# Performance work log

Measured on AMD Instinct MI355X. Metric: run time of the kernel, lower is better.

## Reference

```python
import jax, jax.numpy as jnp
import numpy as np

NEG_SLOPE = 0.01  # F.leaky_relu default


def _unfold3(x):
    # x: [B,C,H,W] -> [B,C,9,H,W] of 3x3 neighborhoods (zero pad 1)
    B, C, H, W = x.shape
    xp = jnp.pad(x, ((0, 0), (0, 0), (1, 1), (1, 1)))
    return jnp.stack([xp[:, :, i:i + H, j:j + W] for i in range(3) for j in range(3)], axis=2)


def _resize_bilinear(img, oh, ow):
    # torch F.interpolate mode='bilinear', align_corners=False, antialias=False
    B, C, H, W = img.shape
    if oh == H and ow == W:
        return img
    def coords(out, inn):
        c = jnp.maximum((jnp.arange(out, dtype=jnp.float32) + 0.5) * (inn / out) - 0.5, 0.0)
        i0 = jnp.floor(c).astype(jnp.int32)
        i1 = jnp.minimum(i0 + 1, inn - 1)
        w = c - i0.astype(jnp.float32)
        return i0, i1, w
    i0, i1, wh = coords(oh, H)
    row = img[:, :, i0, :] * (1.0 - wh)[None, None, :, None] + img[:, :, i1, :] * wh[None, None, :, None]
    j0, j1, ww = coords(ow, W)
    return row[:, :, :, j0] * (1.0 - ww) + row[:, :, :, j1] * ww


def _up2_nearest(x):
    # F.interpolate scale_factor=2 (default mode='nearest')
    return jnp.repeat(jnp.repeat(x, 2, axis=2), 2, axis=3)


def _leaky(x):
    return jnp.where(x >= 0, x, NEG_SLOPE * x)


def _pac_conv(x, guide, w):
    # PacConv2d (gaussian kernel, k=3, stride=1, pad=1, bias=False)
    g_unf = _unfold3(guide)                      # [B,Cg,9,H,W]
    diff = g_unf - guide[:, :, None]             # f_j - f_i
    kern = jnp.exp(-0.5 * jnp.sum(diff * diff, axis=1))  # [B,9,H,W]
    x_unf = _unfold3(x)                          # [B,Ci,9,H,W]
    wk = w.reshape(w.shape[0], w.shape[1], 9)    # [Co,Ci,9]
    return jnp.einsum('oik,bikhw,bkhw->bohw', wk, x_unf, kern)


def setup_inputs() -> dict:
    key = jax.random.key(0)
    ks = jax.random.split(key, 8)
    B, Cx, Hx, Wx = 4, 384, 32, 32
    Hg = Wg = 512
    x = jax.random.normal(ks[0], (B, Cx, Hx, Wx), dtype=jnp.float32)
    guide = jax.random.uniform(ks[1], (B, 3, Hg, Wg), dtype=jnp.float32)
    lin_w = jax.random.normal(ks[2], (16, 384, 1, 1), dtype=jnp.float32) * 0.05
    lin_b = jax.random.normal(ks[3], (16,), dtype=jnp.float32) * 0.05
    chans = [16, 4, 4, 4, 1]
    w0 = jax.random.normal(ks[4], (chans[1], chans[0], 3, 3), dtype=jnp.float32) * 0.1
    w1 = jax.random.normal(ks[5], (chans[2], chans[1], 3, 3), dtype=jnp.float32) * 0.1
    w2 = jax.random.normal(ks[6], (chans[3], chans[2], 3, 3), dtype=jnp.float32) * 0.1
    w3 = jax.random.normal(ks[7], (chans[4], chans[3], 3, 3), dtype=jnp.float32) * 0.1
    return {"x": x, "guide": guide, "lin_w": lin_w, "lin_b": lin_b,
            "w0": w0, "w1": w1, "w2": w2, "w3": w3}


def reference(x, guide, lin_w, lin_b, w0, w1, w2, w3):
    # crop guide to multiple of 16 (module uses shape[-1] for both dims)
    s = (guide.shape[-1] // 16) * 16
    guide = guide[..., :s, :s]
    # 1x1 conv + leaky relu
    x = jnp.einsum('oi,bihw->bohw', lin_w[:, :, 0, 0], x) + lin_b[None, :, None, None]
    x = _leaky(x)
    ws = [w0, w1, w2, w3]
    n = len(ws)
    Hg, Wg = guide.shape[2], guide.shape[3]
    for i in range(n):
        f = 2 ** (n - 1 - i)
        g = _resize_bilinear(guide, Hg // f, Wg // f)
        x = _up2_nearest(x)
        x = _pac_conv(x, g, ws[i])
        if i < n - 1:
            x = _leaky(x)
    return jax.nn.sigmoid(x)
```

## Files before the change

### kernel.cpp

```cpp
#include <hip/hip_runtime.h>
#include <math.h>

#define NEG_SLOPE 0.01f

__device__ inline float bilin(const float* __restrict__ gp, float scale, int r, int c) {
    float ch = fmaxf((r + 0.5f) * scale - 0.5f, 0.f);
    float cw = fmaxf((c + 0.5f) * scale - 0.5f, 0.f);
    int h0 = (int)ch, w0 = (int)cw;
    int h1 = min(h0 + 1, 511), w1 = min(w0 + 1, 511);
    float fh = ch - (float)h0, fw = cw - (float)w0;
    float v00 = gp[h0 * 512 + w0], v01 = gp[h0 * 512 + w1];
    float v10 = gp[h1 * 512 + w0], v11 = gp[h1 * 512 + w1];
    float top = v00 + (v01 - v00) * fw;
    float bot = v10 + (v11 - v10) * fw;
    return top + (bot - top) * fh;
}

__global__ void __launch_bounds__(256)
prep_kernel(const float* __restrict__ x, const float* __restrict__ lw,
            const float* __restrict__ lb, float* __restrict__ x16,
            const float* __restrict__ g, float* __restrict__ g64p,
            float* __restrict__ g128p, float* __restrict__ g256p) {
    int bid = blockIdx.x;
    if (bid < 256) {
        int idx = bid * 256 + threadIdx.x;
        int hw = idx & 1023, co = (idx >> 10) & 15, bb = idx >> 14;
        const float* xp = x + bb * 384 * 1024 + hw;
        const float* wp = lw + co * 384;
        float a0 = 0.f, a1 = 0.f, a2 = 0.f, a3 = 0.f;
        for (int ci = 0; ci < 384; ci += 4) {
            a0 = fmaf(wp[ci],     xp[(ci)     * 1024], a0);
            a1 = fmaf(wp[ci + 1], xp[(ci + 1) * 1024], a1);
            a2 = fmaf(wp[ci + 2], xp[(ci + 2) * 1024], a2);
            a3 = fmaf(wp[ci + 3], xp[(ci + 3) * 1024], a3);
        }
        float acc = lb[co] + ((a0 + a1) + (a2 + a3));
        x16[idx] = acc >= 0.f ? acc : NEG_SLOPE * acc;
    } else {
        int idx = (bid - 256) * 256 + threadIdx.x;
        int R; float scale; float* outp; int o;
        if (idx < 786432)      { R = 256; scale = 2.f; outp = g256p; o = idx; }
        else if (idx < 983040) { R = 128; scale = 4.f; outp = g128p; o = idx - 786432; }
        else                   { R = 64;  scale = 8.f; outp = g64p;  o = idx - 983040; }
        int c = o % R;
        int r = (o / R) % R;
        int bc = o / (R * R);
        outp[o] = bilin(g + (size_t)bc * 262144, scale, r, c);
    }
}

template <int Ci, int Co, int R, int ACT>
__global__ void __launch_bounds__(256)
pac_stage(const float* __restrict__ x, const float* __restrict__ g,
          const float* __restrict__ wk, float* __restrict__ out) {
    __shared__ float sw[Co * Ci * 9];
    for (int i = threadIdx.x; i < Co * Ci * 9; i += 256) sw[i] = wk[i];
    __syncthreads();

    constexpr int HW = R * R;
    constexpr int Rh = R / 2;
    constexpr int HWh = Rh * Rh;
    int idx = blockIdx.x * 256 + threadIdx.x;
    int w = idx & (R - 1);
    int h = (idx / R) & (R - 1);
    int b = idx / HW;

    const float* gb = g + (size_t)b * 3 * HW;
    int ctr = h * R + w;
    float gc0 = gb[ctr];
    float gc1 = gb[HW + ctr];
    float gc2 = gb[2 * HW + ctr];

    float acc[Co];
#pragma unroll
    for (int co = 0; co < Co; ++co) acc[co] = 0.f;

    const float* xb = x + (size_t)b * Ci * HWh;

#pragma unroll
    for (int t = 0; t < 9; ++t) {
        int dh = t / 3 - 1, dw = t % 3 - 1;
        int hh = h + dh, ww = w + dw;
        if (hh < 0 || hh >= R || ww < 0 || ww >= R) continue;
        int tap = hh * R + ww;
        float d0 = gb[tap] - gc0;
        float d1 = gb[HW + tap] - gc1;
        float d2 = gb[2 * HW + tap] - gc2;
        float k = __expf(-0.5f * (d0 * d0 + d1 * d1 + d2 * d2));
        const float* xp = xb + (hh >> 1) * Rh + (ww >> 1);
#pragma unroll
        for (int ci = 0; ci < Ci; ++ci) {
            float xv = xp[ci * HWh] * k;
#pragma unroll
            for (int co = 0; co < Co; ++co)
                acc[co] = fmaf(sw[(co * Ci + ci) * 9 + t], xv, acc[co]);
        }
    }

#pragma unroll
    for (int co = 0; co < Co; ++co) {
        float v = acc[co];
        if (ACT == 0) v = v >= 0.f ? v : NEG_SLOPE * v;
        else          v = 1.0f / (1.0f + __expf(-v));
        out[(size_t)(b * Co + co) * HW + ctr] = v;
    }
}

template <int Ci, int Co>
__device__ inline void pac_lds(const float* __restrict__ sx, int BXr, int BXc, int NX,
                               const float* __restrict__ sg, int BGr, int BGc, int NG,
                               const float* __restrict__ sw, float* __restrict__ so,
                               int BOr, int BOc, int NO, int RES) {
    const int NG2 = NG * NG, NX2 = NX * NX, NO2 = NO * NO;
    for (int i = threadIdx.x; i < NO2; i += 256) {
        int r = i / NO, c = i % NO;
        int gh = BOr + r, gw = BOc + c;
        float acc[Co];
#pragma unroll
        for (int co = 0; co < Co; ++co) acc[co] = 0.f;
        if (gh >= 0 && gh < RES && gw >= 0 && gw < RES) {
            int lc0 = (gh - BGr) * NG + (gw - BGc);
            float gc0 = sg[lc0], gc1 = sg[NG2 + lc0], gc2 = sg[2 * NG2 + lc0];
#pragma unroll
            for (int tt = 0; tt < 9; ++tt) {
                int hh = gh + tt / 3 - 1, ww = gw + tt % 3 - 1;
                if (hh < 0 || hh >= RES || ww < 0 || ww >= RES) continue;
                int lt = (hh - BGr) * NG + (ww - BGc);
                float d0 = sg[lt] - gc0;
                float d1 = sg[NG2 + lt] - gc1;
                float d2 = sg[2 * NG2 + lt] - gc2;
                float k = __expf(-0.5f * (d0 * d0 + d1 * d1 + d2 * d2));
                int lx = ((hh >> 1) - BXr) * NX + ((ww >> 1) - BXc);
#pragma unroll
                for (int ci = 0; ci < Ci; ++ci) {
                    float xv = sx[ci * NX2 + lx] * k;
#pragma unroll
                    for (int co = 0; co < Co; ++co)
                        acc[co] = fmaf(sw[(co * Ci + ci) * 9 + tt], xv, acc[co]);
                }
            }
        }
#pragma unroll
        for (int co = 0; co < Co; ++co) {
            float v = acc[co];
            so[co * NO2 + i] = v >= 0.f ? v : NEG_SLOPE * v;
        }
    }
}

__global__ void __launch_bounds__(256)
pac_tail_kernel(const float* __restrict__ x1g, const float* __restrict__ guide,
                const float* __restrict__ g256p,
                const float* __restrict__ w2, const float* __restrict__ w3,
                float* __restrict__ out) {
    __shared__ float smem[6544];
    float* sw2   = smem;
    float* sw3   = smem + 144;
    float* sg512 = smem + 180;
    float* sg256 = smem + 3648;
    float* sx1   = smem + 4848;
    float* sx2   = smem + 5248;

    int bid = blockIdx.x;
    int xcd = bid & 7;
    int j   = bid >> 3;
    int b    = xcd >> 1;
    int half = xcd & 1;
    int t = half * 8 + (j >> 4);
    int u = j & 15;

    const int B1r = 8 * t - 1,   B1c = 8 * u - 1;
    const int BG2r = 16 * t - 2, BG2c = 16 * u - 2;
    const int B2r = 16 * t - 1,  B2c = 16 * u - 1;
    const int BG3r = 32 * t - 1, BG3c = 32 * u - 1;

    const float* gb = guide + (size_t)b * 3 * 262144;

    for (int i = threadIdx.x; i < 3468; i += 256) {
        int ch = i / 1156, rem = i % 1156, r = rem / 34, c = rem % 34;
        int gr = BG3r + r, gc = BG3c + c;
        float v = 0.f;
        if (gr >= 0 && gr < 512 && gc >= 0 && gc < 512)
            v = gb[ch * 262144 + (gr << 9) + gc];
        sg512[i] = v;
    }
    for (int i = threadIdx.x; i < 1200; i += 256) {
        int ch = i / 400, rem = i % 400, r = rem / 20, c = rem % 20;
        int gr = BG2r + r, gc = BG2c + c;
        float v = 0.f;
        if (gr >= 0 && gr < 256 && gc >= 0 && gc < 256)
            v = g256p[(b * 3 + ch) * 65536 + (gr << 8) + gc];
        sg256[i] = v;
    }
    for (int i = threadIdx.x; i < 400; i += 256) {
        int ci = i / 100, rem = i % 100, r = rem / 10, c = rem % 10;
        int gr = B1r + r, gc = B1c + c;
        float v = 0.f;
        if (gr >= 0 && gr < 128 && gc >= 0 && gc < 128)
            v = x1g[((b * 4 + ci) << 14) + (gr << 7) + gc];
        sx1[i] = v;
    }
    for (int i = threadIdx.x; i < 144; i += 256) sw2[i] = w2[i];
    for (int i = threadIdx.x; i < 36;  i += 256) sw3[i] = w3[i];
    __syncthreads();

    pac_lds<4, 4>(sx1, B1r, B1c, 10, sg256, BG2r, BG2c, 20, sw2, sx2, B2r, B2c, 18, 256);
    __syncthreads();

    float* ob = out + (size_t)b * 262144;
    for (int i = threadIdx.x; i < 1024; i += 256) {
        int r = i >> 5, c = i & 31;
        int gh = 32 * t + r, gw = 32 * u + c;
        int lc0 = (gh - BG3r) * 34 + (gw - BG3c);
        float gc0 = sg512[lc0], gc1 = sg512[1156 + lc0], gc2 = sg512[2 * 1156 + lc0];
        float acc = 0.f;
#pragma unroll
        for (int tt = 0; tt < 9; ++tt) {
            int hh = gh + tt / 3 - 1, ww = gw + tt % 3 - 1;
            if (hh < 0 || hh >= 512 || ww < 0 || ww >= 512) continue;
            int lt = (hh - BG3r) * 34 + (ww - BG3c);
            float d0 = sg512[lt] - gc0;
            float d1 = sg512[1156 + lt] - gc1;
            float d2 = sg512[2 * 1156 + lt] - gc2;
            float k = __expf(-0.5f * (d0 * d0 + d1 * d1 + d2 * d2));
            int lx = ((hh >> 1) - B2r) * 18 + ((ww >> 1) - B2c);
#pragma unroll
            for (int ci = 0; ci < 4; ++ci)
                acc = fmaf(sw3[ci * 9 + tt], sx2[ci * 324 + lx] * k, acc);
        }
        ob[(gh << 9) + gw] = 1.0f / (1.0f + __expf(-acc));
    }
}

extern "C" void kernel_launch(void* const* d_in, const int* in_sizes, int n_in,
                              void* d_out, int out_size, void* d_ws, size_t ws_size,
                              hipStream_t stream) {
    const float* x     = (const float*)d_in[0];
    const float* guide = (const float*)d_in[1];
    const float* lin_w = (const float*)d_in[2];
    const float* lin_b = (const float*)d_in[3];
    const float* w0    = (const float*)d_in[4];
    const float* w1    = (const float*)d_in[5];
    const float* w2    = (const float*)d_in[6];
    const float* w3    = (const float*)d_in[7];
    float* out = (float*)d_out;

    float* ws    = (float*)d_ws;
    float* x16   = ws;
    float* g64p  = x16 + 65536;
    float* g128p = g64p + 49152;
    float* g256p = g128p + 196608;
    float* x0    = g256p + 786432;
    float* x1    = x0 + 65536;

    prep_kernel<<<4288, 256, 0, stream>>>(x, lin_w, lin_b, x16, guide, g64p, g128p, g256p);
    pac_stage<16, 4, 64, 0><<<64, 256, 0, stream>>>(x16, g64p, w0, x0);
    pac_stage<4, 4, 128, 0><<<256, 256, 0, stream>>>(x0, g128p, w1, x1);
    pac_tail_kernel<<<1024, 256, 0, stream>>>(x1, guide, g256p, w2, w3, out);
}
```

Measured before the change: 134.7 us.

## Fuse stages 0-1 into tiled kernel, unfuse tail into stage2 plus quad-pixel 512 kernel

Stages 0 and 1 are merged into one LDS-tiled kernel with halo recompute, which removes a launch and the round trip of the stage-0 activation through global memory. The former fused stage2+stage3 tail kernel is split into a plain pac_stage for the 256-resolution layer and a new register-blocked kernel where each thread computes a 2x2 output quad from a 4x4 guide window and a 3x3 x window held in registers. This trades the LDS halo recompute and shared-memory traffic of the tail for an extra global write and read of the 256x256 intermediate.

```diff
diff --git a/kernel.cpp b/kernel.cpp
--- a/kernel.cpp
+++ b/kernel.cpp
@@ -49,6 +49,136 @@
     }
 }
 
+template <int Ci, int Co>
+__device__ inline void pac_lds(const float* __restrict__ sx, int BXr, int BXc, int NX,
+                               const float* __restrict__ sg, int BGr, int BGc, int NG,
+                               const float* __restrict__ sw, float* __restrict__ so,
+                               int BOr, int BOc, int NO, int RES) {
+    const int NG2 = NG * NG, NX2 = NX * NX, NO2 = NO * NO;
+    for (int i = threadIdx.x; i < NO2; i += 256) {
+        int r = i / NO, c = i % NO;
+        int gh = BOr + r, gw = BOc + c;
+        float acc[Co];
+#pragma unroll
+        for (int co = 0; co < Co; ++co) acc[co] = 0.f;
+        if (gh >= 0 && gh < RES && gw >= 0 && gw < RES) {
+            int lc0 = (gh - BGr) * NG + (gw - BGc);
+            float gc0 = sg[lc0], gc1 = sg[NG2 + lc0], gc2 = sg[2 * NG2 + lc0];
+#pragma unroll
+            for (int tt = 0; tt < 9; ++tt) {
+                int hh = gh + tt / 3 - 1, ww = gw + tt % 3 - 1;
+                if (hh < 0 || hh >= RES || ww < 0 || ww >= RES) continue;
+                int lt = (hh - BGr) * NG + (ww - BGc);
+                float d0 = sg[lt] - gc0;
+                float d1 = sg[NG2 + lt] - gc1;
+                float d2 = sg[2 * NG2 + lt] - gc2;
+                float k = __expf(-0.5f * (d0 * d0 + d1 * d1 + d2 * d2));
+                int lx = ((hh >> 1) - BXr) * NX + ((ww >> 1) - BXc);
+#pragma unroll
+                for (int ci = 0; ci < Ci; ++ci) {
+                    float xv = sx[ci * NX2 + lx] * k;
+#pragma unroll
+                    for (int co = 0; co < Co; ++co)
+                        acc[co] = fmaf(sw[(co * Ci + ci) * 9 + tt], xv, acc[co]);
+                }
+            }
+        }
+#pragma unroll
+        for (int co = 0; co < Co; ++co) {
+            float v = acc[co];
+            so[co * NO2 + i] = v >= 0.f ? v : NEG_SLOPE * v;
+        }
+    }
+}
+
+__global__ void __launch_bounds__(256)
+pac_mid_kernel(const float* __restrict__ x16g, const float* __restrict__ g64p,
+               const float* __restrict__ g128p,
+               const float* __restrict__ w0, const float* __restrict__ w1,
+               float* __restrict__ x1g) {
+    __shared__ float smem[3100];
+    float* sw0   = smem;
+    float* sw1   = smem + 576;
+    float* sx16  = smem + 720;
+    float* sg64  = smem + 1296;
+    float* sg128 = smem + 1728;
+    float* sx0   = smem + 2700;
+
+    int bid = blockIdx.x;
+    int b = bid >> 6;
+    int t = (bid >> 3) & 7;
+    int u = bid & 7;
+
+    const int BXr = 4 * t - 1,  BXc = 4 * u - 1;
+    const int BG0r = 8 * t - 2, BG0c = 8 * u - 2;
+    const int B0r = 8 * t - 1,  B0c = 8 * u - 1;
+    const int BG1r = 16 * t - 1, BG1c = 16 * u - 1;
+
+    for (int i = threadIdx.x; i < 576; i += 256) sw0[i] = w0[i];
+    for (int i = threadIdx.x; i < 144; i += 256) sw1[i] = w1[i];
+    for (int i = threadIdx.x; i < 576; i += 256) {
+        int ci = i / 36, rem = i % 36, r = rem / 6, c = rem % 6;
+        int gr = BXr + r, gc = BXc + c;
+        float v = 0.f;
+        if (gr >= 0 && gr < 32 && gc >= 0 && gc < 32)
+            v = x16g[((b * 16 + ci) << 10) + (gr << 5) + gc];
+        sx16[i] = v;
+    }
+    for (int i = threadIdx.x; i < 432; i += 256) {
+        int ch = i / 144, rem = i % 144, r = rem / 12, c = rem % 12;
+        int gr = BG0r + r, gc = BG0c + c;
+        float v = 0.f;
+        if (gr >= 0 && gr < 64 && gc >= 0 && gc < 64)
+            v = g64p[(b * 3 + ch) * 4096 + (gr << 6) + gc];
+        sg64[i] = v;
+    }
+    for (int i = threadIdx.x; i < 972; i += 256) {
+        int ch = i / 324, rem = i % 324, r = rem / 18, c = rem % 18;
+        int gr = BG1r + r, gc = BG1c + c;
+        float v = 0.f;
+        if (gr >= 0 && gr < 128 && gc >= 0 && gc < 128)
+            v = g128p[(b * 3 + ch) * 16384 + (gr << 7) + gc];
+        sg128[i] = v;
+    }
+    __syncthreads();
+
+    pac_lds<16, 4>(sx16, BXr, BXc, 6, sg64, BG0r, BG0c, 12, sw0, sx0, B0r, B0c, 10, 64);
+    __syncthreads();
+
+    {
+        int i = threadIdx.x;
+        int r = i >> 4, c = i & 15;
+        int gh = 16 * t + r, gw = 16 * u + c;
+        int lc0 = (gh - BG1r) * 18 + (gw - BG1c);
+        float gc0 = sg128[lc0], gc1 = sg128[324 + lc0], gc2 = sg128[648 + lc0];
+        float acc[4] = {0.f, 0.f, 0.f, 0.f};
+#pragma unroll
+        for (int tt = 0; tt < 9; ++tt) {
+            int hh = gh + tt / 3 - 1, ww = gw + tt % 3 - 1;
+            if (hh < 0 || hh >= 128 || ww < 0 || ww >= 128) continue;
+            int lt = (hh - BG1r) * 18 + (ww - BG1c);
+            float d0 = sg128[lt] - gc0;
+            float d1 = sg128[324 + lt] - gc1;
+            float d2 = sg128[648 + lt] - gc2;
+            float k = __expf(-0.5f * (d0 * d0 + d1 * d1 + d2 * d2));
+            int lx = ((hh >> 1) - B0r) * 10 + ((ww >> 1) - B0c);
+#pragma unroll
+            for (int ci = 0; ci < 4; ++ci) {
+                float xv = sx0[ci * 100 + lx] * k;
+#pragma unroll
+                for (int co = 0; co < 4; ++co)
+                    acc[co] = fmaf(sw1[(co * 4 + ci) * 9 + tt], xv, acc[co]);
+            }
+        }
+#pragma unroll
+        for (int co = 0; co < 4; ++co) {
+            float v = acc[co];
+            v = v >= 0.f ? v : NEG_SLOPE * v;
+            x1g[((b * 4 + co) << 14) + (gh << 7) + gw] = v;
+        }
+    }
+}
+
 template <int Ci, int Co, int R, int ACT>
 __global__ void __launch_bounds__(256)
 pac_stage(const float* __restrict__ x, const float* __restrict__ g,
@@ -106,129 +236,79 @@
     }
 }
 
-template <int Ci, int Co>
-__device__ inline void pac_lds(const float* __restrict__ sx, int BXr, int BXc, int NX,
-                               const float* __restrict__ sg, int BGr, int BGc, int NG,
-                               const float* __restrict__ sw, float* __restrict__ so,
-                               int BOr, int BOc, int NO, int RES) {
-    const int NG2 = NG * NG, NX2 = NX * NX, NO2 = NO * NO;
-    for (int i = threadIdx.x; i < NO2; i += 256) {
-        int r = i / NO, c = i % NO;
-        int gh = BOr + r, gw = BOc + c;
-        float acc[Co];
-#pragma unroll
-        for (int co = 0; co < Co; ++co) acc[co] = 0.f;
-        if (gh >= 0 && gh < RES && gw >= 0 && gw < RES) {
-            int lc0 = (gh - BGr) * NG + (gw - BGc);
-            float gc0 = sg[lc0], gc1 = sg[NG2 + lc0], gc2 = sg[2 * NG2 + lc0];
+__global__ void __launch_bounds__(256)
+pac512_quad_kernel(const float* __restrict__ x2g, const float* __restrict__ guide,
+                   const float* __restrict__ w3, float* __restrict__ out) {
+    __shared__ float sw[36];
+    if (threadIdx.x < 36) sw[threadIdx.x] = w3[threadIdx.x];
+    __syncthreads();
+
+    int idx = blockIdx.x * 256 + threadIdx.x;
+    int qw = idx & 255;
+    int qh = (idx >> 8) & 255;
+    int b = idx >> 16;
+    int h0 = qh << 1, w0 = qw << 1;
+
+    const float* gb = guide + (size_t)b * 3 * 262144;
+    const float* xb = x2g + (size_t)b * 4 * 65536;
+
+    float gw[3][4][4];
+#pragma unroll
+    for (int rr = 0; rr < 4; ++rr) {
+        int gr = h0 - 1 + rr;
+        bool rok = (gr >= 0 && gr < 512);
+#pragma unroll
+        for (int cc = 0; cc < 4; ++cc) {
+            int gc = w0 - 1 + cc;
+            bool ok = rok && (gc >= 0 && gc < 512);
+            int a = (gr << 9) + gc;
+#pragma unroll
+            for (int ch = 0; ch < 3; ++ch)
+                gw[ch][rr][cc] = ok ? gb[ch * 262144 + a] : 0.f;
+        }
+    }
+    float xw[4][3][3];
+#pragma unroll
+    for (int rr = 0; rr < 3; ++rr) {
+        int xr = qh - 1 + rr;
+        bool rok = (xr >= 0 && xr < 256);
+#pragma unroll
+        for (int cc = 0; cc < 3; ++cc) {
+            int xc = qw - 1 + cc;
+            bool ok = rok && (xc >= 0 && xc < 256);
+            int a = (xr << 8) + xc;
+#pragma unroll
+            for (int ci = 0; ci < 4; ++ci)
+                xw[ci][rr][cc] = ok ? xb[ci * 65536 + a] : 0.f;
+        }
+    }
+
+    float* ob = out + (size_t)b * 262144;
+#pragma unroll
+    for (int dr = 0; dr < 2; ++dr) {
+#pragma unroll
+        for (int dc = 0; dc < 2; ++dc) {
+            float gc0 = gw[0][dr + 1][dc + 1];
+            float gc1 = gw[1][dr + 1][dc + 1];
+            float gc2 = gw[2][dr + 1][dc + 1];
+            float acc = 0.f;
 #pragma unroll
             for (int tt = 0; tt < 9; ++tt) {
-                int hh = gh + tt / 3 - 1, ww = gw + tt % 3 - 1;
-                if (hh < 0 || hh >= RES || ww < 0 || ww >= RES) continue;
-                int lt = (hh - BGr) * NG + (ww - BGc);
-                float d0 = sg[lt] - gc0;
-                float d1 = sg[NG2 + lt] - gc1;
-                float d2 = sg[2 * NG2 + lt] - gc2;
+                const int th = tt / 3, tc = tt % 3;
+                int hh = h0 + dr + th - 1, ww = w0 + dc + tc - 1;
+                if (hh < 0 || hh >= 512 || ww < 0 || ww >= 512) continue;
+                float d0 = gw[0][dr + th][dc + tc] - gc0;
+                float d1 = gw[1][dr + th][dc + tc] - gc1;
+                float d2 = gw[2][dr + th][dc + tc] - gc2;
                 float k = __expf(-0.5f * (d0 * d0 + d1 * d1 + d2 * d2));
-                int lx = ((hh >> 1) - BXr) * NX + ((ww >> 1) - BXc);
-#pragma unroll
-                for (int ci = 0; ci < Ci; ++ci) {
-                    float xv = sx[ci * NX2 + lx] * k;
-#pragma unroll
-                    for (int co = 0; co < Co; ++co)
-                        acc[co] = fmaf(sw[(co * Ci + ci) * 9 + tt], xv, acc[co]);
-                }
+                const int xr = ((dr + th - 1) >> 1) + 1;
+                const int xc = ((dc + tc - 1) >> 1) + 1;
+#pragma unroll
+                for (int ci = 0; ci < 4; ++ci)
+                    acc = fmaf(sw[ci * 9 + tt], xw[ci][xr][xc] * k, acc);
             }
-        }
-#pragma unroll
-        for (int co = 0; co < Co; ++co) {
-            float v = acc[co];
-            so[co * NO2 + i] = v >= 0.f ? v : NEG_SLOPE * v;
-        }
-    }
-}
-
-__global__ void __launch_bounds__(256)
-pac_tail_kernel(const float* __restrict__ x1g, const float* __restrict__ guide,
-                const float* __restrict__ g256p,
-                const float* __restrict__ w2, const float* __restrict__ w3,
-                float* __restrict__ out) {
-    __shared__ float smem[6544];
-    float* sw2   = smem;
-    float* sw3   = smem + 144;
-    float* sg512 = smem + 180;
-    float* sg256 = smem + 3648;
-    float* sx1   = smem + 4848;
-    float* sx2   = smem + 5248;
-
-    int bid = blockIdx.x;
-    int xcd = bid & 7;
-    int j   = bid >> 3;
-    int b    = xcd >> 1;
-    int half = xcd & 1;
-    int t = half * 8 + (j >> 4);
-    int u = j & 15;
-
-    const int B1r = 8 * t - 1,   B1c = 8 * u - 1;
-    const int BG2r = 16 * t - 2, BG2c = 16 * u - 2;
-    const int B2r = 16 * t - 1,  B2c = 16 * u - 1;
-    const int BG3r = 32 * t - 1, BG3c = 32 * u - 1;
-
-    const float* gb = guide + (size_t)b * 3 * 262144;
-
-    for (int i = threadIdx.x; i < 3468; i += 256) {
-        int ch = i / 1156, rem = i % 1156, r = rem / 34, c = rem % 34;
-        int gr = BG3r + r, gc = BG3c + c;
-        float v = 0.f;
-        if (gr >= 0 && gr < 512 && gc >= 0 && gc < 512)
-            v = gb[ch * 262144 + (gr << 9) + gc];
-        sg512[i] = v;
-    }
-    for (int i = threadIdx.x; i < 1200; i += 256) {
-        int ch = i / 400, rem = i % 400, r = rem / 20, c = rem % 20;
-        int gr = BG2r + r, gc = BG2c + c;
-        float v = 0.f;
-        if (gr >= 0 && gr < 256 && gc >= 0 && gc < 256)
-            v = g256p[(b * 3 + ch) * 65536 + (gr << 8) + gc];
-        sg256[i] = v;
-    }
-    for (int i = threadIdx.x; i < 400; i += 256) {
-        int ci = i / 100, rem = i % 100, r = rem / 10, c = rem % 10;
-        int gr = B1r + r, gc = B1c + c;
-        float v = 0.f;
-        if (gr >= 0 && gr < 128 && gc >= 0 && gc < 128)
-            v = x1g[((b * 4 + ci) << 14) + (gr << 7) + gc];
-        sx1[i] = v;
-    }
-    for (int i = threadIdx.x; i < 144; i += 256) sw2[i] = w2[i];
-    for (int i = threadIdx.x; i < 36;  i += 256) sw3[i] = w3[i];
-    __syncthreads();
-
-    pac_lds<4, 4>(sx1, B1r, B1c, 10, sg256, BG2r, BG2c, 20, sw2, sx2, B2r, B2c, 18, 256);
-    __syncthreads();
-
-    float* ob = out + (size_t)b * 262144;
-    for (int i = threadIdx.x; i < 1024; i += 256) {
-        int r = i >> 5, c = i & 31;
-        int gh = 32 * t + r, gw = 32 * u + c;
-        int lc0 = (gh - BG3r) * 34 + (gw - BG3c);
-        float gc0 = sg512[lc0], gc1 = sg512[1156 + lc0], gc2 = sg512[2 * 1156 + lc0];
-        float acc = 0.f;
-#pragma unroll
-        for (int tt = 0; tt < 9; ++tt) {
-            int hh = gh + tt / 3 - 1, ww = gw + tt % 3 - 1;
-            if (hh < 0 || hh >= 512 || ww < 0 || ww >= 512) continue;
-            int lt = (hh - BG3r) * 34 + (ww - BG3c);
-            float d0 = sg512[lt] - gc0;
-            float d1 = sg512[1156 + lt] - gc1;
-            float d2 = sg512[2 * 1156 + lt] - gc2;
-            float k = __expf(-0.5f * (d0 * d0 + d1 * d1 + d2 * d2));
-            int lx = ((hh >> 1) - B2r) * 18 + ((ww >> 1) - B2c);
-#pragma unroll
-            for (int ci = 0; ci < 4; ++ci)
-                acc = fmaf(sw3[ci * 9 + tt], sx2[ci * 324 + lx] * k, acc);
-        }
-        ob[(gh << 9) + gw] = 1.0f / (1.0f + __expf(-acc));
+            ob[((h0 + dr) << 9) + (w0 + dc)] = 1.0f / (1.0f + __expf(-acc));
+        }
     }
 }
 
@@ -250,11 +330,11 @@
     float* g64p  = x16 + 65536;
     float* g128p = g64p + 49152;
     float* g256p = g128p + 196608;
-    float* x0    = g256p + 786432;
-    float* x1    = x0 + 65536;
+    float* x1    = g256p + 786432;
+    float* x2    = x1 + 262144;
 
     prep_kernel<<<4288, 256, 0, stream>>>(x, lin_w, lin_b, x16, guide, g64p, g128p, g256p);
-    pac_stage<16, 4, 64, 0><<<64, 256, 0, stream>>>(x16, g64p, w0, x0);
-    pac_stage<4, 4, 128, 0><<<256, 256, 0, stream>>>(x0, g128p, w1, x1);
-    pac_tail_kernel<<<1024, 256, 0, stream>>>(x1, guide, g256p, w2, w3, out);
-}
+    pac_mid_kernel<<<256, 256, 0, stream>>>(x16, g64p, g128p, w0, w1, x1);
+    pac_stage<4, 4, 256, 0><<<1024, 256, 0, stream>>>(x1, g256p, w2, x2);
+    pac512_quad_kernel<<<1024, 256, 0, stream>>>(x2, guide, w3, out);
+}
```

Result: faster. 120.0 us (-10.9%).
